# Kernel tuning notes

Measured on AMD Instinct MI355X. Metric: run time of the kernel, lower is better.

Reference implementation:

```python
import jax, jax.numpy as jnp
import numpy as np

D_MODEL = 1024
NHEAD = 16
DK = D_MODEL // NHEAD
B, LQ, LK = 4, 2048, 2048


def setup_inputs() -> dict:
    key = jax.random.key(0)
    ks = jax.random.split(key, 11)
    s = 1.0 / np.sqrt(D_MODEL)
    inp = {
        "q": jax.random.normal(ks[0], (B, LQ, D_MODEL), jnp.float32),
        "k": jax.random.normal(ks[1], (B, LK, D_MODEL), jnp.float32),
        "v": jax.random.normal(ks[2], (B, LK, D_MODEL), jnp.float32),
        "attn_mask": jnp.triu(jnp.ones((LQ, LK), dtype=bool), k=1),  # True = masked (causal)
        "Wq": jax.random.normal(ks[3], (D_MODEL, D_MODEL), jnp.float32) * s,
        "bq": jnp.zeros((D_MODEL,), jnp.float32),
        "Wk": jax.random.normal(ks[4], (D_MODEL, D_MODEL), jnp.float32) * s,
        "bk": jnp.zeros((D_MODEL,), jnp.float32),
        "Wv": jax.random.normal(ks[5], (D_MODEL, D_MODEL), jnp.float32) * s,
        "bv": jnp.zeros((D_MODEL,), jnp.float32),
        "Wo": jax.random.normal(ks[6], (D_MODEL, D_MODEL), jnp.float32) * s,
        "bo": jnp.zeros((D_MODEL,), jnp.float32),
    }
    return inp


def _split_heads(x, L):
    # (B, L, D) -> (B, H, L, dk)
    return x.reshape(B, L, NHEAD, DK).transpose(0, 2, 1, 3)


def reference(q, k, v, attn_mask, Wq, bq, Wk, bk, Wv, bv, Wo, bo):
    qh = _split_heads(q @ Wq + bq, LQ)
    kh = _split_heads(k @ Wk + bk, LK)
    vh = _split_heads(v @ Wv + bv, LK)
    scale = 1.0 / np.sqrt(DK).astype(np.float32)
    scores = jnp.einsum("bhqd,bhkd->bhqk", qh, kh) * scale
    scores = jnp.where(attn_mask[None, None, :, :], -jnp.inf, scores)
    attn = jax.nn.softmax(scores, axis=-1)
    ctx = jnp.einsum("bhqk,bhkd->bhqd", attn, vh)
    ctx = ctx.transpose(0, 2, 1, 3).reshape(B, LQ, D_MODEL)
    return ctx @ Wo + bo
```

## Files before the change

### kernel.cpp

```cpp
#include <hip/hip_runtime.h>

#define D_MODEL 1024
#define NHEAD 16
#define DKH 64
#define BATCH 4
#define SEQ 2048
#define MROWS (BATCH*SEQ)

typedef unsigned short u16;
typedef __attribute__((ext_vector_type(8))) short bf16x8;
typedef __attribute__((ext_vector_type(4))) float f32x4;

__device__ __forceinline__ u16 f2bf(float f) {
  union { float f; unsigned int u; } x; x.f = f;
  unsigned int r = x.u + 0x7FFFu + ((x.u >> 16) & 1u);
  return (u16)(r >> 16);
}
__device__ __forceinline__ u16 f2bf_fast(float f) {
  union { float f; unsigned int u; } x; x.f = f;
  return (u16)((x.u + 0x7FFFu) >> 16);
}

__device__ __forceinline__ f32x4 mfma16(bf16x8 a, bf16x8 b, f32x4 c) {
  return __builtin_amdgcn_mfma_f32_16x16x32_bf16(a, b, c, 0, 0, 0);
}

__device__ __forceinline__ void gld_lds16(const void* g, void* l) {
  __builtin_amdgcn_global_load_lds((const __attribute__((address_space(1))) unsigned int*)g,
                                   (__attribute__((address_space(3))) unsigned int*)l, 16, 0, 0);
}

__global__ __launch_bounds__(256) void transpose_cvt4(
    const float* __restrict__ W0, const float* __restrict__ W1,
    const float* __restrict__ W2, const float* __restrict__ W3,
    u16* __restrict__ T0, u16* __restrict__ T1,
    u16* __restrict__ T2, u16* __restrict__ T3) {
  const int z = blockIdx.z;
  const float* W = (z == 0) ? W0 : (z == 1) ? W1 : (z == 2) ? W2 : W3;
  u16* Wt = (z == 0) ? T0 : (z == 1) ? T1 : (z == 2) ? T2 : T3;
  __shared__ float tile[32][33];
  int bx = blockIdx.x * 32, by = blockIdx.y * 32;
  int tx = threadIdx.x, ty = threadIdx.y;
#pragma unroll
  for (int j = 0; j < 32; j += 8)
    tile[ty + j][tx] = W[(size_t)(by + ty + j) * D_MODEL + bx + tx];
  __syncthreads();
#pragma unroll
  for (int j = 0; j < 32; j += 8)
    Wt[(size_t)(bx + ty + j) * D_MODEL + by + tx] = f2bf(tile[tx][ty + j]);
}

template <typename Epi>
__device__ __forceinline__ void gemm_pipe_f32a(const float* __restrict__ Ap32,
                                               const u16* __restrict__ Bp,
                                               int m0, int n0g, Epi epi) {
  __shared__ u16 As[2][128 * 64];
  __shared__ u16 Bs[2][128 * 64];
  const int tid = threadIdx.x;
  const int lane = tid & 63;
  const int w = tid >> 6;
  const int wm = w >> 1, wn = w & 1;
  const int lo = lane & 15, g = lane >> 4;
  const int swz = (lo & 7) << 4;
  const int sg = (tid & 7) ^ ((tid >> 3) & 7);
  const int srow = tid >> 3;

  f32x4 acc[4][4] = {};
  float4 ar[8];

  auto LOAD_A = [&](int tt) {
#pragma unroll
    for (int j = 0; j < 4; ++j) {
      const float* p = Ap32 + (size_t)(m0 + j * 32 + srow) * D_MODEL + tt * 64 + sg * 8;
      ar[2 * j] = *(const float4*)p;
      ar[2 * j + 1] = *(const float4*)(p + 4);
    }
  };
  auto WRITE_A = [&](int buf) {
#pragma unroll
    for (int j = 0; j < 4; ++j) {
      bf16x8 t;
      t[0] = (short)f2bf(ar[2 * j].x); t[1] = (short)f2bf(ar[2 * j].y);
      t[2] = (short)f2bf(ar[2 * j].z); t[3] = (short)f2bf(ar[2 * j].w);
      t[4] = (short)f2bf(ar[2 * j + 1].x); t[5] = (short)f2bf(ar[2 * j + 1].y);
      t[6] = (short)f2bf(ar[2 * j + 1].z); t[7] = (short)f2bf(ar[2 * j + 1].w);
      *(bf16x8*)&As[buf][j * 2048 + tid * 8] = t;
    }
  };
  auto STAGE_B = [&](int buf, int tt) {
#pragma unroll
    for (int j = 0; j < 4; ++j)
      gld_lds16(Bp + (size_t)(n0g + j * 32 + srow) * D_MODEL + tt * 64 + sg * 8,
                &Bs[buf][j * 2048 + tid * 8]);
  };

  LOAD_A(0);
  STAGE_B(0, 0);
  STAGE_B(1, 1);
  asm volatile("s_waitcnt vmcnt(8)" ::: "memory");
  WRITE_A(0);
  asm volatile("s_waitcnt vmcnt(4)" ::: "memory");
  asm volatile("s_waitcnt lgkmcnt(0)" ::: "memory");
  __builtin_amdgcn_s_barrier();

  int cur = 0;
#pragma unroll 1
  for (int t = 0; t < 16; ++t) {
    const int nb = cur ^ 1;
    const char* ab = (const char*)&As[cur][0];
    const char* bb2 = (const char*)&Bs[cur][0];

    bf16x8 bf[4][2], af[2][2];
#pragma unroll
    for (int n = 0; n < 4; ++n) {
      int row = wn * 64 + n * 16 + lo;
      bf[n][0] = *(const bf16x8*)(bb2 + row * 128 + ((g * 16) ^ swz));
      bf[n][1] = *(const bf16x8*)(bb2 + row * 128 + ((64 + g * 16) ^ swz));
    }
#pragma unroll
    for (int m = 0; m < 2; ++m) {
      int row = wm * 64 + m * 16 + lo;
      af[m][0] = *(const bf16x8*)(ab + row * 128 + ((g * 16) ^ swz));
      af[m][1] = *(const bf16x8*)(ab + row * 128 + ((64 + g * 16) ^ swz));
    }
    if (t + 1 < 16) LOAD_A(t + 1);
    __builtin_amdgcn_s_barrier();
    __builtin_amdgcn_s_setprio(1);
#pragma unroll
    for (int s2 = 0; s2 < 2; ++s2)
#pragma unroll
      for (int m = 0; m < 2; ++m)
#pragma unroll
        for (int n = 0; n < 4; ++n)
          acc[m][n] = mfma16(af[m][s2], bf[n][s2], acc[m][n]);
    __builtin_amdgcn_s_setprio(0);
    __builtin_amdgcn_s_barrier();

    bf16x8 af2[2][2];
#pragma unroll
    for (int m = 0; m < 2; ++m) {
      int row = wm * 64 + (m + 2) * 16 + lo;
      af2[m][0] = *(const bf16x8*)(ab + row * 128 + ((g * 16) ^ swz));
      af2[m][1] = *(const bf16x8*)(ab + row * 128 + ((64 + g * 16) ^ swz));
    }
    if (t + 2 < 16) STAGE_B(cur, t + 2);
    __builtin_amdgcn_s_barrier();
    __builtin_amdgcn_s_setprio(1);
#pragma unroll
    for (int s2 = 0; s2 < 2; ++s2)
#pragma unroll
      for (int m = 0; m < 2; ++m)
#pragma unroll
        for (int n = 0; n < 4; ++n)
          acc[m + 2][n] = mfma16(af2[m][s2], bf[n][s2], acc[m + 2][n]);
    __builtin_amdgcn_s_setprio(0);
    if (t + 1 < 16) {
      if (t + 2 < 16) asm volatile("s_waitcnt vmcnt(4)" ::: "memory");
      else            asm volatile("s_waitcnt vmcnt(0)" ::: "memory");
      WRITE_A(nb);
      asm volatile("s_waitcnt lgkmcnt(0)" ::: "memory");
      __builtin_amdgcn_s_barrier();
    }
    cur = nb;
  }

  epi(acc, wm, wn, lo, g);
}

template <typename Epi>
__device__ __forceinline__ void gemm_pipe(const u16* __restrict__ Ap,
                                          const u16* __restrict__ Bp,
                                          int m0, int n0g, Epi epi) {
  __shared__ u16 As[2][128 * 64];
  __shared__ u16 Bs[2][128 * 64];
  const int tid = threadIdx.x;
  const int lane = tid & 63;
  const int w = tid >> 6;
  const int wm = w >> 1, wn = w & 1;
  const int lo = lane & 15, g = lane >> 4;
  const int swz = (lo & 7) << 4;
  const int sg = (tid & 7) ^ ((tid >> 3) & 7);
  const int srow = tid >> 3;

  f32x4 acc[4][4] = {};

  auto STAGE_A = [&](int buf, int tt, int j) {
    int row = j * 32 + srow;
    gld_lds16(Ap + (size_t)(m0 + row) * D_MODEL + tt * 64 + sg * 8,
              &As[buf][j * 2048 + tid * 8]);
  };
  auto STAGE_B = [&](int buf, int tt, int j) {
    int row = j * 32 + srow;
    gld_lds16(Bp + (size_t)(n0g + row) * D_MODEL + tt * 64 + sg * 8,
              &Bs[buf][j * 2048 + tid * 8]);
  };

  STAGE_A(0, 0, 0); STAGE_A(0, 0, 1); STAGE_A(0, 0, 2); STAGE_A(0, 0, 3);
  STAGE_B(0, 0, 0); STAGE_B(0, 0, 1); STAGE_B(0, 0, 2); STAGE_B(0, 0, 3);
  STAGE_B(1, 1, 0); STAGE_B(1, 1, 1); STAGE_B(1, 1, 2); STAGE_B(1, 1, 3);
  asm volatile("s_waitcnt vmcnt(4)" ::: "memory");
  __builtin_amdgcn_s_barrier();

  int cur = 0;
#pragma unroll 1
  for (int t = 0; t < 16; ++t) {
    const int nb = cur ^ 1;
    const char* ab = (const char*)&As[cur][0];
    const char* bb2 = (const char*)&Bs[cur][0];

    bf16x8 bf[4][2], af[2][2];
#pragma unroll
    for (int n = 0; n < 4; ++n) {
      int row = wn * 64 + n * 16 + lo;
      bf[n][0] = *(const bf16x8*)(bb2 + row * 128 + ((g * 16) ^ swz));
      bf[n][1] = *(const bf16x8*)(bb2 + row * 128 + ((64 + g * 16) ^ swz));
    }
#pragma unroll
    for (int m = 0; m < 2; ++m) {
      int row = wm * 64 + m * 16 + lo;
      af[m][0] = *(const bf16x8*)(ab + row * 128 + ((g * 16) ^ swz));
      af[m][1] = *(const bf16x8*)(ab + row * 128 + ((64 + g * 16) ^ swz));
    }
    if (t + 1 < 16) {
      STAGE_A(nb, t + 1, 0); STAGE_A(nb, t + 1, 1);
      STAGE_A(nb, t + 1, 2); STAGE_A(nb, t + 1, 3);
    }
    __builtin_amdgcn_s_barrier();
    __builtin_amdgcn_s_setprio(1);
#pragma unroll
    for (int s2 = 0; s2 < 2; ++s2)
#pragma unroll
      for (int m = 0; m < 2; ++m)
#pragma unroll
        for (int n = 0; n < 4; ++n)
          acc[m][n] = mfma16(af[m][s2], bf[n][s2], acc[m][n]);
    __builtin_amdgcn_s_setprio(0);
    __builtin_amdgcn_s_barrier();

    bf16x8 af2[2][2];
#pragma unroll
    for (int m = 0; m < 2; ++m) {
      int row = wm * 64 + (m + 2) * 16 + lo;
      af2[m][0] = *(const bf16x8*)(ab + row * 128 + ((g * 16) ^ swz));
      af2[m][1] = *(const bf16x8*)(ab + row * 128 + ((64 + g * 16) ^ swz));
    }
    if (t + 2 < 16) {
      STAGE_B(cur, t + 2, 0); STAGE_B(cur, t + 2, 1);
      STAGE_B(cur, t + 2, 2); STAGE_B(cur, t + 2, 3);
    }
    __builtin_amdgcn_s_barrier();
    __builtin_amdgcn_s_setprio(1);
#pragma unroll
    for (int s2 = 0; s2 < 2; ++s2)
#pragma unroll
      for (int m = 0; m < 2; ++m)
#pragma unroll
        for (int n = 0; n < 4; ++n)
          acc[m + 2][n] = mfma16(af2[m][s2], bf[n][s2], acc[m + 2][n]);
    __builtin_amdgcn_s_setprio(0);
    if (t + 2 < 16) asm volatile("s_waitcnt vmcnt(4)" ::: "memory");
    else            asm volatile("s_waitcnt vmcnt(0)" ::: "memory");
    __builtin_amdgcn_s_barrier();
    cur = nb;
  }

  epi(acc, wm, wn, lo, g);
}

__global__ __launch_bounds__(256, 2) void gemm_qkv_kernel(
    const float* __restrict__ Aq, const float* __restrict__ Ak, const float* __restrict__ Av,
    const u16* __restrict__ Wt,
    const float* __restrict__ bq, const float* __restrict__ bk, const float* __restrict__ bv,
    u16* __restrict__ Qhd, u16* __restrict__ Khd, u16* __restrict__ Vhd, float qscale) {
  const int flat = blockIdx.x;
  const int swzb = (flat & 7) * 192 + (flat >> 3);
  const int m0 = (swzb / 24) * 128;
  const int n0g = (swzb % 24) * 128;
  const int chunk = n0g >> 10;
  const float* Ap = (chunk == 0) ? Aq : (chunk == 1) ? Ak : Av;
  const float* bias = (chunk == 0) ? bq : (chunk == 1) ? bk : bv;
  const float scale = (chunk == 0) ? qscale : 1.0f;

  gemm_pipe_f32a(Ap, Wt, m0, n0g,
    [&](f32x4 (&acc)[4][4], int wm, int wn, int lo, int g) {
#pragma unroll
      for (int m = 0; m < 4; ++m)
#pragma unroll
        for (int n = 0; n < 4; ++n) {
          int row0 = m0 + wm * 64 + m * 16 + g * 4;
          int colc = (n0g & 1023) + wn * 64 + n * 16 + lo;
          int hh = colc >> 6, d = colc & 63;
          int bb = row0 >> 11;
          float v0 = (acc[m][n][0] + bias[colc]) * scale;
          float v1 = (acc[m][n][1] + bias[colc]) * scale;
          float v2 = (acc[m][n][2] + bias[colc]) * scale;
          float v3 = (acc[m][n][3] + bias[colc]) * scale;
          if (chunk < 2) {
            u16* out = chunk ? Khd : Qhd;
#pragma unroll
            for (int i = 0; i < 4; ++i) {
              int l = (row0 + i) & 2047;
              float vi = (i == 0) ? v0 : (i == 1) ? v1 : (i == 2) ? v2 : v3;
              out[(((size_t)(bb * NHEAD + hh)) * SEQ + l) * DKH + d] = f2bf(vi);
            }
          } else {
            int l = row0 & 2047;
            int kh = (l >> 2) & 7;
            int pos = (l & ~31) | ((2 * (kh & 3) + (kh >> 2)) << 2);
            ushort4 o;
            o.x = f2bf(v0); o.y = f2bf(v1); o.z = f2bf(v2); o.w = f2bf(v3);
            *(ushort4*)&Vhd[(((size_t)(bb * NHEAD + hh)) * DKH + d) * SEQ + pos] = o;
          }
        }
    });
}

__global__ __launch_bounds__(256, 2) void gemm_o_kernel(
    const u16* __restrict__ A, const u16* __restrict__ Bt,
    const float* __restrict__ bias, float* __restrict__ Cout) {
  const int flat = blockIdx.x;
  const int swzb = (flat & 7) * 64 + (flat >> 3);
  const int m0 = (swzb >> 3) * 128;
  const int n0g = (swzb & 7) * 128;

  gemm_pipe(A, Bt, m0, n0g,
    [&](f32x4 (&acc)[4][4], int wm, int wn, int lo, int g) {
#pragma unroll
      for (int m = 0; m < 4; ++m)
#pragma unroll
        for (int n = 0; n < 4; ++n) {
          int row0 = m0 + wm * 64 + m * 16 + g * 4;
          int col = n0g + wn * 64 + n * 16 + lo;
          float bcol = bias[col];
#pragma unroll
          for (int i = 0; i < 4; ++i)
            Cout[(size_t)(row0 + i) * D_MODEL + col] = acc[m][n][i] + bcol;
        }
    });
}

__global__ __launch_bounds__(256, 3) void attn_kernel(
    const u16* __restrict__ Qh, const u16* __restrict__ Kh,
    const u16* __restrict__ Vt, u16* __restrict__ ctx) {
  const int blk = blockIdx.x;
  const int xcd = blk & 7;
  const int local = blk >> 3;
  const int qb = 15 - (local >> 3);
  const int head = xcd * 8 + (local & 7);
  const int b = head >> 4, h = head & (NHEAD - 1);

  const int tid = threadIdx.x;
  const int lane = tid & 63;
  const int w = tid >> 6;
  const int lo = lane & 15, g = lane >> 4;
  const int swz = (lo & 7) << 4;

  __shared__ u16 Ks[3][64 * 64];
  __shared__ u16 Vs[3][64 * 64];

  const size_t hoff = ((size_t)(b * NHEAD + h)) * SEQ * DKH;
  const u16* Qp = Qh + hoff;
  const u16* Kp = Kh + hoff;
  const u16* Vp = Vt + hoff;

  const int nt = 2 * qb + 2;
  const int qmin = qb * 128 + w * 32;

  bf16x8 aq[2][2];
#pragma unroll
  for (int qs = 0; qs < 2; ++qs)
#pragma unroll
    for (int cc = 0; cc < 2; ++cc)
      aq[qs][cc] = *(const bf16x8*)(Qp + (size_t)(qmin + qs * 16 + lo) * DKH + cc * 32 + g * 8);

  const int r_lo = lane >> 3;
  const int sgr = (lane & 7) ^ r_lo;

  auto STAGE = [&](int buf, int t64) {
#pragma unroll
    for (int j = 0; j < 2; ++j) {
      int row = w * 16 + j * 8 + r_lo;
      gld_lds16(Kp + (size_t)(t64 * 64 + row) * DKH + sgr * 8, &Ks[buf][(w * 2 + j) * 512]);
      gld_lds16(Vp + (size_t)row * SEQ + t64 * 64 + sgr * 8, &Vs[buf][(w * 2 + j) * 512]);
    }
  };

  STAGE(0, 0);
  STAGE(1, 1);
  asm volatile("s_waitcnt vmcnt(0)" ::: "memory");
  __builtin_amdgcn_s_barrier();

  f32x4 c[2][4] = {};
  float m_run[2] = {-1e30f, -1e30f}, l_run[2] = {0.f, 0.f};
  int cur = 0;

  for (int kt = 0; kt < nt; ++kt) {
    int b2 = cur + 2; if (b2 >= 3) b2 -= 3;
    if (kt + 2 < nt) STAGE(b2, kt + 2);

    f32x4 s[2][4] = {};
#pragma unroll
    for (int kn = 0; kn < 4; ++kn) {
      const char* krow = (const char*)&Ks[cur][(kn * 16 + lo) * 64];
#pragma unroll
      for (int cc = 0; cc < 2; ++cc) {
        bf16x8 ak = *(const bf16x8*)(krow + ((cc * 64 + g * 16) ^ swz));
        s[0][kn] = mfma16(ak, aq[0][cc], s[0][kn]);
        s[1][kn] = mfma16(ak, aq[1][cc], s[1][kn]);
      }
    }

    if (kt >= nt - 2) {
#pragma unroll
      for (int qs = 0; qs < 2; ++qs) {
        int q = qmin + qs * 16 + lo;
#pragma unroll
        for (int kn = 0; kn < 4; ++kn)
#pragma unroll
          for (int i = 0; i < 4; ++i) {
            int key = kt * 64 + kn * 16 + g * 4 + i;
            if (key > q) s[qs][kn][i] = -1e30f;
          }
      }
    }

    bf16x8 pb[2][2];
#pragma unroll
    for (int qs = 0; qs < 2; ++qs) {
      float mx = s[qs][0][0];
#pragma unroll
      for (int kn = 0; kn < 4; ++kn)
#pragma unroll
        for (int i = 0; i < 4; ++i) mx = fmaxf(mx, s[qs][kn][i]);
      mx = fmaxf(mx, __shfl_xor(mx, 16));
      mx = fmaxf(mx, __shfl_xor(mx, 32));
      if (!__all(mx - m_run[qs] <= 8.0f)) {
        float mnew = fmaxf(m_run[qs], mx);
        float al = __builtin_amdgcn_exp2f(m_run[qs] - mnew);
        m_run[qs] = mnew;
        l_run[qs] *= al;
#pragma unroll
        for (int dn = 0; dn < 4; ++dn) {
          c[qs][dn][0] *= al; c[qs][dn][1] *= al;
          c[qs][dn][2] *= al; c[qs][dn][3] *= al;
        }
      }
      const float mq = m_run[qs];
      float rs = 0.f;
#pragma unroll
      for (int kn = 0; kn < 4; ++kn)
#pragma unroll
        for (int i = 0; i < 4; ++i) {
          float p = __builtin_amdgcn_exp2f(s[qs][kn][i] - mq);
          s[qs][kn][i] = p;
          rs += p;
        }
      rs += __shfl_xor(rs, 16);
      rs += __shfl_xor(rs, 32);
      l_run[qs] += rs;
#pragma unroll
      for (int kc = 0; kc < 2; ++kc) {
        bf16x8 t;
        t[0] = (short)f2bf_fast(s[qs][2 * kc][0]);
        t[1] = (short)f2bf_fast(s[qs][2 * kc][1]);
        t[2] = (short)f2bf_fast(s[qs][2 * kc][2]);
        t[3] = (short)f2bf_fast(s[qs][2 * kc][3]);
        t[4] = (short)f2bf_fast(s[qs][2 * kc + 1][0]);
        t[5] = (short)f2bf_fast(s[qs][2 * kc + 1][1]);
        t[6] = (short)f2bf_fast(s[qs][2 * kc + 1][2]);
        t[7] = (short)f2bf_fast(s[qs][2 * kc + 1][3]);
        pb[qs][kc] = t;
      }
    }

#pragma unroll
    for (int kc = 0; kc < 2; ++kc)
#pragma unroll
      for (int dn = 0; dn < 4; ++dn) {
        const char* vrow = (const char*)&Vs[cur][(dn * 16 + lo) * 64];
        bf16x8 av = *(const bf16x8*)(vrow + ((kc * 64 + g * 16) ^ swz));
        c[0][dn] = mfma16(av, pb[0][kc], c[0][dn]);
        c[1][dn] = mfma16(av, pb[1][kc], c[1][dn]);
      }

    if (kt + 1 < nt) {
      if (kt + 2 < nt) asm volatile("s_waitcnt vmcnt(4)" ::: "memory");
      else             asm volatile("s_waitcnt vmcnt(0)" ::: "memory");
      __builtin_amdgcn_s_barrier();
    }
    cur = (cur == 2) ? 0 : cur + 1;
  }

#pragma unroll
  for (int qs = 0; qs < 2; ++qs) {
    const float rl = 1.0f / l_run[qs];
    const int q = qmin + qs * 16 + lo;
#pragma unroll
    for (int dn = 0; dn < 4; ++dn) {
      ushort4 o;
      o.x = f2bf(c[qs][dn][0] * rl);
      o.y = f2bf(c[qs][dn][1] * rl);
      o.z = f2bf(c[qs][dn][2] * rl);
      o.w = f2bf(c[qs][dn][3] * rl);
      *(ushort4*)&ctx[((size_t)(b * SEQ + q)) * D_MODEL + h * DKH + dn * 16 + g * 4] = o;
    }
  }
}

extern "C" void kernel_launch(void* const* d_in, const int* in_sizes, int n_in,
                              void* d_out, int out_size, void* d_ws, size_t ws_size,
                              hipStream_t stream) {
  const float* q  = (const float*)d_in[0];
  const float* k  = (const float*)d_in[1];
  const float* v  = (const float*)d_in[2];
  const float* Wq = (const float*)d_in[4];
  const float* bq = (const float*)d_in[5];
  const float* Wk = (const float*)d_in[6];
  const float* bk = (const float*)d_in[7];
  const float* Wv = (const float*)d_in[8];
  const float* bv = (const float*)d_in[9];
  const float* Wo = (const float*)d_in[10];
  const float* bo = (const float*)d_in[11];

  char* ws = (char*)d_ws;
  const size_t MB = 1u << 20;
  u16* ctxb = (u16*)(ws + 0 * MB);
  u16* Wqkvt = (u16*)(ws + 48 * MB);
  u16* Wot  = (u16*)(ws + 54 * MB);
  u16* Qhd  = (u16*)(ws + 56 * MB);
  u16* Khd  = (u16*)(ws + 72 * MB);
  u16* Vhd  = (u16*)(ws + 88 * MB);

  u16* Wqt = Wqkvt;
  u16* Wkt = Wqkvt + 1024 * 1024;
  u16* Wvt = Wqkvt + 2 * 1024 * 1024;
  transpose_cvt4<<<dim3(32, 32, 4), dim3(32, 8), 0, stream>>>(
      Wq, Wk, Wv, Wo, Wqt, Wkt, Wvt, Wot);

  const float qscale = 0.125f * 1.4426950408889634f;
  gemm_qkv_kernel<<<1536, 256, 0, stream>>>(q, k, v, Wqkvt,
                                            bq, bk, bv, Qhd, Khd, Vhd, qscale);

  attn_kernel<<<1024, 256, 0, stream>>>(Qhd, Khd, Vhd, ctxb);

  gemm_o_kernel<<<512, 256, 0, stream>>>(ctxb, Wot, bo, (float*)d_out);
}
```

Baseline: 175.5 us.

## Double-buffer fp32 A prefetch in registers and use packed bf16 convert

The fp32-A GEMM path now holds two register sets of A loads, prefetching two k-tiles ahead instead of one, and moves the LDS write of the next A tile earlier, between the two MFMA halves. The per-element manual bf16 rounding is replaced by the hardware v_cvt_pk_bf16_f32 instruction. The aim is to hide global load latency for the projection inputs and cut conversion ALU work. It costs more VGPRs, which may lower occupancy, and the new vmcnt accounting has to match the interleaved outstanding loads exactly.

```diff
diff --git a/kernel.cpp b/kernel.cpp
--- a/kernel.cpp
+++ b/kernel.cpp
@@ -66,26 +66,43 @@
   const int srow = tid >> 3;
 
   f32x4 acc[4][4] = {};
-  float4 ar[8];
-
-  auto LOAD_A = [&](int tt) {
+  float4 a0r[8], a1r[8];
+
+  auto LOAD_A0 = [&](int tt) {
 #pragma unroll
     for (int j = 0; j < 4; ++j) {
       const float* p = Ap32 + (size_t)(m0 + j * 32 + srow) * D_MODEL + tt * 64 + sg * 8;
-      ar[2 * j] = *(const float4*)p;
-      ar[2 * j + 1] = *(const float4*)(p + 4);
-    }
-  };
-  auto WRITE_A = [&](int buf) {
+      a0r[2 * j] = *(const float4*)p;
+      a0r[2 * j + 1] = *(const float4*)(p + 4);
+    }
+  };
+  auto LOAD_A1 = [&](int tt) {
 #pragma unroll
     for (int j = 0; j < 4; ++j) {
-      bf16x8 t;
-      t[0] = (short)f2bf(ar[2 * j].x); t[1] = (short)f2bf(ar[2 * j].y);
-      t[2] = (short)f2bf(ar[2 * j].z); t[3] = (short)f2bf(ar[2 * j].w);
-      t[4] = (short)f2bf(ar[2 * j + 1].x); t[5] = (short)f2bf(ar[2 * j + 1].y);
-      t[6] = (short)f2bf(ar[2 * j + 1].z); t[7] = (short)f2bf(ar[2 * j + 1].w);
-      *(bf16x8*)&As[buf][j * 2048 + tid * 8] = t;
-    }
+      const float* p = Ap32 + (size_t)(m0 + j * 32 + srow) * D_MODEL + tt * 64 + sg * 8;
+      a1r[2 * j] = *(const float4*)p;
+      a1r[2 * j + 1] = *(const float4*)(p + 4);
+    }
+  };
+  auto PACK8 = [&](const float4& u, const float4& v) {
+    unsigned int p0, p1, p2, p3;
+    asm("v_cvt_pk_bf16_f32 %0, %1, %2" : "=v"(p0) : "v"(u.x), "v"(u.y));
+    asm("v_cvt_pk_bf16_f32 %0, %1, %2" : "=v"(p1) : "v"(u.z), "v"(u.w));
+    asm("v_cvt_pk_bf16_f32 %0, %1, %2" : "=v"(p2) : "v"(v.x), "v"(v.y));
+    asm("v_cvt_pk_bf16_f32 %0, %1, %2" : "=v"(p3) : "v"(v.z), "v"(v.w));
+    union { unsigned int q[4]; bf16x8 v8; } r;
+    r.q[0] = p0; r.q[1] = p1; r.q[2] = p2; r.q[3] = p3;
+    return r.v8;
+  };
+  auto WRITE_A0 = [&](int buf) {
+#pragma unroll
+    for (int j = 0; j < 4; ++j)
+      *(bf16x8*)&As[buf][j * 2048 + tid * 8] = PACK8(a0r[2 * j], a0r[2 * j + 1]);
+  };
+  auto WRITE_A1 = [&](int buf) {
+#pragma unroll
+    for (int j = 0; j < 4; ++j)
+      *(bf16x8*)&As[buf][j * 2048 + tid * 8] = PACK8(a1r[2 * j], a1r[2 * j + 1]);
   };
   auto STAGE_B = [&](int buf, int tt) {
 #pragma unroll
@@ -94,18 +111,19 @@
                 &Bs[buf][j * 2048 + tid * 8]);
   };
 
-  LOAD_A(0);
+  LOAD_A0(0);
+  LOAD_A1(1);
   STAGE_B(0, 0);
   STAGE_B(1, 1);
-  asm volatile("s_waitcnt vmcnt(8)" ::: "memory");
-  WRITE_A(0);
+  asm volatile("s_waitcnt vmcnt(16)" ::: "memory");
+  WRITE_A0(0);
   asm volatile("s_waitcnt vmcnt(4)" ::: "memory");
   asm volatile("s_waitcnt lgkmcnt(0)" ::: "memory");
   __builtin_amdgcn_s_barrier();
 
-  int cur = 0;
 #pragma unroll 1
   for (int t = 0; t < 16; ++t) {
+    const int cur = t & 1;
     const int nb = cur ^ 1;
     const char* ab = (const char*)&As[cur][0];
     const char* bb2 = (const char*)&Bs[cur][0];
@@ -123,7 +141,9 @@
       af[m][0] = *(const bf16x8*)(ab + row * 128 + ((g * 16) ^ swz));
       af[m][1] = *(const bf16x8*)(ab + row * 128 + ((64 + g * 16) ^ swz));
     }
-    if (t + 1 < 16) LOAD_A(t + 1);
+    if (t + 2 < 16) {
+      if (t & 1) LOAD_A1(t + 2); else LOAD_A0(t + 2);
+    }
     __builtin_amdgcn_s_barrier();
     __builtin_amdgcn_s_setprio(1);
 #pragma unroll
@@ -136,6 +156,11 @@
     __builtin_amdgcn_s_setprio(0);
     __builtin_amdgcn_s_barrier();
 
+    if (t + 1 < 16) {
+      if (t + 2 < 16) asm volatile("s_waitcnt vmcnt(12)" ::: "memory");
+      else            asm volatile("s_waitcnt vmcnt(4)" ::: "memory");
+      if (t & 1) WRITE_A0(nb); else WRITE_A1(nb);
+    }
     bf16x8 af2[2][2];
 #pragma unroll
     for (int m = 0; m < 2; ++m) {
@@ -155,13 +180,11 @@
           acc[m + 2][n] = mfma16(af2[m][s2], bf[n][s2], acc[m + 2][n]);
     __builtin_amdgcn_s_setprio(0);
     if (t + 1 < 16) {
-      if (t + 2 < 16) asm volatile("s_waitcnt vmcnt(4)" ::: "memory");
+      if (t + 2 < 16) asm volatile("s_waitcnt vmcnt(12)" ::: "memory");
       else            asm volatile("s_waitcnt vmcnt(0)" ::: "memory");
-      WRITE_A(nb);
       asm volatile("s_waitcnt lgkmcnt(0)" ::: "memory");
       __builtin_amdgcn_s_barrier();
     }
-    cur = nb;
   }
 
   epi(acc, wm, wn, lo, g);
```

After: 192.0 us. +9.4%, slower.
